# Kernel optimization log

Hardware: AMD Instinct MI355X
Metric: run time of the kernel (lower is better)

## Reference

```python
import jax, jax.numpy as jnp
import numpy as np

NUM_HEADS = 8
EPS = 1e-5  # torch GroupNorm default eps


def setup_inputs() -> dict:
    key = jax.random.key(0)
    ks = jax.random.split(key, 3)
    B, C, H, W = 8, 384, 32, 32
    x = jax.random.normal(ks[0], (B, C, H, W), dtype=jnp.float32)
    qkv_w = jax.random.normal(ks[1], (3 * C, C), dtype=jnp.float32) * 0.02
    proj_w = jax.random.normal(ks[2], (C, C), dtype=jnp.float32) * 0.02
    proj_b = jnp.zeros((C,), dtype=jnp.float32)
    lambda_param = jnp.ones((1, NUM_HEADS, 1, 1), dtype=jnp.float32) * 0.5
    gc = NUM_HEADS * ((C // NUM_HEADS) // 2)  # 192 group-norm channels
    gn_weight = jnp.ones((gc,), dtype=jnp.float32)
    gn_bias = jnp.zeros((gc,), dtype=jnp.float32)
    return {"x": x, "qkv_w": qkv_w, "lambda_param": lambda_param,
            "gn_weight": gn_weight, "gn_bias": gn_bias,
            "proj_w": proj_w, "proj_b": proj_b}


def reference(x, qkv_w, lambda_param, gn_weight, gn_bias, proj_w, proj_b):
    B, C, H, W = x.shape
    nh = NUM_HEADS
    hd = C // nh
    hd2 = hd // 2
    N = H * W
    scale = hd ** -0.5

    xf = x.reshape(B, C, N)
    qkv = jnp.einsum('oc,bcn->bon', qkv_w, xf)  # (B, 3C, N), 1x1 conv no bias
    q, k, v = jnp.split(qkv, 3, axis=1)
    q = q.reshape(B, nh, hd, N)
    k = k.reshape(B, nh, hd, N)
    v = v.reshape(B, nh, hd, N)

    q1, q2 = q[:, :, :hd2], q[:, :, hd2:]
    k1, k2 = k[:, :, :hd2], k[:, :, hd2:]
    v1, v2 = v[:, :, :hd2], v[:, :, hd2:]

    # GroupNorm(2 groups) on q2 viewed as (B, nh*hd2, H, W)
    gc = nh * hd2
    qg = q2.reshape(B, 2, (gc // 2) * N)  # normalize over (group channels, H, W)
    mean = qg.mean(axis=2, keepdims=True)
    var = qg.var(axis=2, keepdims=True)
    qg = (qg - mean) * jax.lax.rsqrt(var + EPS)
    q2n = qg.reshape(B, gc, N) * gn_weight[None, :, None] + gn_bias[None, :, None]
    q2n = q2n.reshape(B, nh, hd2, N)

    # dual softmax attention maps (B, nh, N, N)
    attn1 = jax.nn.softmax(jnp.einsum('bhdn,bhdm->bhnm', q1, k1) * scale, axis=-1)
    attn2 = jax.nn.softmax(jnp.einsum('bhdn,bhdm->bhnm', q2n, k2) * scale * lambda_param, axis=-1)
    diff = attn1 - attn2

    out1 = jnp.einsum('bhnm,bhdm->bhnd', diff, v1)  # (B, nh, N, hd2)
    out2 = jnp.einsum('bhnm,bhdm->bhnd', diff, v2)
    out = jnp.concatenate([out1, out2], axis=2)  # (B, nh, 2N, hd2) -- matches torch cat dim=2
    out = out.reshape(B, C, H, W)

    out = jnp.einsum('oc,bchw->bohw', proj_w, out) + proj_b[None, :, None, None]
    return out
```

## Files before the change

kernel.cpp:

```cpp
#include <hip/hip_runtime.h>
#include <hip/hip_bf16.h>
#include <stdint.h>

typedef _Float16 half8 __attribute__((ext_vector_type(8)));
typedef _Float16 half4 __attribute__((ext_vector_type(4)));
typedef __fp16 fp16x2 __attribute__((ext_vector_type(2)));
typedef float floatx4 __attribute__((ext_vector_type(4)));
typedef float floatx16 __attribute__((ext_vector_type(16)));

#define SCALE 0.14433756729740643f
#define LOG2E 1.4426950408889634f


__device__ inline float fexp2(float x) { return __builtin_exp2f(x); }

__device__ inline uint32_t pkrtz(float a, float b) {
  fp16x2 h = __builtin_amdgcn_cvt_pkrtz(a, b);
  union { fp16x2 h; uint32_t u; } cv; cv.h = h; return cv.u;
}

__global__ void k_pack(const float* __restrict__ src, _Float16* __restrict__ dst, int nchunks) {
  int cid = blockIdx.x * 256 + threadIdx.x;
  if (cid >= nchunks) return;
  int lane = cid & 63;
  int t = cid >> 6;
  int cb = t % 12;
  int g16 = t / 12;
  const float* s = src + (long)(g16 * 16 + (lane & 15)) * 384 + cb * 32 + (lane >> 4) * 8;
  floatx4 a = *(const floatx4*)s;
  floatx4 b = *(const floatx4*)(s + 4);
  half8 h;
  #pragma unroll
  for (int j = 0; j < 4; j++) { h[j] = (_Float16)a[j]; h[j+4] = (_Float16)b[j]; }
  *(half8*)(dst + (long)cid * 8) = h;
}

__launch_bounds__(256)
__global__ void k_tr(const float* __restrict__ src, _Float16* __restrict__ dst) {
  const int cblk = blockIdx.x, nseg = blockIdx.y, b = blockIdx.z;
  const float* S = src + ((long)b * 384 + cblk * 32) * 1024 + nseg * 256;
  _Float16* D = dst + (long)b * 393216 + cblk * 32768 + (long)nseg * 256 * 32;
  __shared__ _Float16 T[32][264];
  const int wv = threadIdx.x >> 6, lane = threadIdx.x & 63;
  #pragma unroll
  for (int rr = 0; rr < 8; rr++) {
    int r = wv * 8 + rr;
    floatx4 v = *(const floatx4*)(S + (long)r * 1024 + lane * 4);
    half4 h;
    #pragma unroll
    for (int j = 0; j < 4; j++) h[j] = (_Float16)v[j];
    *(half4*)&T[r][lane * 4] = h;
  }
  __syncthreads();
  const int nn = threadIdx.x >> 3, c = (threadIdx.x & 7) * 4;
  #pragma unroll
  for (int p = 0; p < 8; p++) {
    int n = p * 32 + nn;
    half4 h;
    #pragma unroll
    for (int i = 0; i < 4; i++) h[i] = T[c + i][n];
    *(half4*)(D + (long)n * 32 + c) = h;
  }
}

__launch_bounds__(256, 4)
__global__ void k_qkv(const _Float16* __restrict__ Xt, const _Float16* __restrict__ Wf,
                      _Float16* __restrict__ Qs, _Float16* __restrict__ Ks,
                      _Float16* __restrict__ Vs) {
  const int tid = threadIdx.x;
  const int lane = tid & 63;
  const int wv = tid >> 6;
  const int l15 = lane & 15;
  const int g = lane >> 4;
  const int o0 = blockIdx.x * 48;
  const int n0 = blockIdx.y * 64;
  const int b = blockIdx.z;

  const int ncol = n0 + wv * 16 + l15;
  const _Float16* xp = Xt + (long)b * 393216 + (long)ncol * 32 + g * 8;
  const _Float16* wfb = Wf + (long)(blockIdx.x * 36) * 512 + lane * 8;

  half8 xb[12];
  #pragma unroll
  for (int cb = 0; cb < 12; cb++) xb[cb] = *(const half8*)(xp + cb * 32768);

  floatx4 zero4 = {0.f, 0.f, 0.f, 0.f};
  floatx4 acc0 = zero4, acc1 = zero4, acc2 = zero4;

  half8 A0 = *(const half8*)(wfb);
  half8 A1 = *(const half8*)(wfb + 12 * 512);
  half8 A2 = *(const half8*)(wfb + 24 * 512);
  #pragma unroll
  for (int cb = 0; cb < 12; cb++) {
    half8 c0 = A0, c1 = A1, c2 = A2;
    if (cb < 11) {
      A0 = *(const half8*)(wfb + (cb + 1) * 512);
      A1 = *(const half8*)(wfb + (12 + cb + 1) * 512);
      A2 = *(const half8*)(wfb + (24 + cb + 1) * 512);
    }
    acc0 = __builtin_amdgcn_mfma_f32_16x16x32_f16(c0, xb[cb], acc0, 0, 0, 0);
    acc1 = __builtin_amdgcn_mfma_f32_16x16x32_f16(c1, xb[cb], acc1, 0, 0, 0);
    acc2 = __builtin_amdgcn_mfma_f32_16x16x32_f16(c2, xb[cb], acc2, 0, 0, 0);
  }

  floatx4 acc[3] = {acc0, acc1, acc2};
  __shared__ __align__(16) _Float16 T[3456];

  if (o0 < 768) {
    #pragma unroll
    for (int rt = 0; rt < 3; rt++)
      #pragma unroll
      for (int r = 0; r < 4; r++)
        T[(wv * 16 + l15) * 52 + rt * 16 + g * 4 + r] = (_Float16)acc[rt][r];
    __syncthreads();
    const int qk = o0 >= 384;
    const int hh = (o0 - qk * 384) / 48;
    _Float16* base = (qk ? Ks : Qs) + (long)(b * 8 + hh) * 65536;
    #pragma unroll
    for (int it = 0; it < 2; it++) {
      int slot = it * 256 + tid;
      int ntl = slot >> 8;
      int t   = (slot >> 6) & 3;
      int ln  = slot & 63;
      int hi_s = ln >> 5, l31_s = ln & 31;
      int n_ = ntl * 32 + l31_s;
      int c0 = t * 16 + hi_s * 8;
      half8 val;
      #pragma unroll
      for (int j = 0; j < 8; j++) {
        int col = c0 + j;
        int d48 = col < 24 ? col : col - 8;
        bool isq = (col < 24) || (col >= 32 && col < 56);
        val[j] = isq ? T[n_ * 52 + d48] : (_Float16)0;
      }
      *(half8*)(base + ((((n0 >> 5) + ntl) * 4 + t) * 64 + ln) * 8) = val;
    }
  } else {
    #pragma unroll
    for (int rt = 0; rt < 3; rt++)
      #pragma unroll
      for (int r = 0; r < 4; r++)
        T[(rt * 16 + g * 4 + r) * 72 + wv * 16 + l15] = (_Float16)acc[rt][r];
    __syncthreads();
    const int hh = (o0 - 768) / 48;
    _Float16* base = Vs + (long)(b * 8 + hh) * 65536;
    #pragma unroll
    for (int it = 0; it < 2; it++) {
      int slot = it * 256 + tid;
      int lwin = slot >> 8;
      int ckc  = (slot >> 6) & 3;
      int kc   = ckc & 1, c = ckc >> 1;
      int ln = slot & 63;
      int hi_s = ln >> 5, l31_s = ln & 31;
      int d48 = c * 32 + l31_s;
      half8 val;
      if (d48 < 48) {
        int mb = lwin * 32 + kc * 16 + hi_s * 4;
        half4 a = *(const half4*)&T[d48 * 72 + mb];
        half4 bq = *(const half4*)&T[d48 * 72 + mb + 8];
        val[0] = a[0]; val[1] = a[1]; val[2] = a[2]; val[3] = a[3];
        val[4] = bq[0]; val[5] = bq[1]; val[6] = bq[2]; val[7] = bq[3];
      } else {
        _Float16 f = (d48 == 48) ? (_Float16)1 : (_Float16)0;
        #pragma unroll
        for (int j = 0; j < 8; j++) val[j] = f;
      }
      *(half8*)(base + ((((n0 >> 5) + lwin) * 4 + ckc) * 64 + ln) * 8) = val;
    }
  }
}

__global__ void k_gnstats(const _Float16* __restrict__ Qs, float* __restrict__ partial) {
  int bg = blockIdx.x >> 3;
  int chunk = blockIdx.x & 7;
  int b = bg >> 1, grp = bg & 1;
  float s1 = 0.f, s2 = 0.f;
  #pragma unroll
  for (int k = 0; k < 6; k++) {
    int f = chunk * 1536 + k * 256 + threadIdx.x;
    int uid = f / 96;
    int slot = f - uid * 96;
    int h = grp * 4 + (uid >> 5);
    int ntile = uid & 31;
    int t = slot < 64 ? 2 : 3;
    int ln = slot < 64 ? slot : slot - 64;
    const _Float16* p = Qs + (long)(b * 8 + h) * 65536 + ((ntile * 4 + t) * 64 + ln) * 8;
    half8 v = *(const half8*)p;
    #pragma unroll
    for (int j = 0; j < 8; j++) { float x = (float)v[j]; s1 += x; s2 += x * x; }
  }
  #pragma unroll
  for (int off = 32; off > 0; off >>= 1) {
    s1 += __shfl_down(s1, off);
    s2 += __shfl_down(s2, off);
  }
  __shared__ float red[8];
  int wv = threadIdx.x >> 6;
  if ((threadIdx.x & 63) == 0) { red[wv] = s1; red[4 + wv] = s2; }
  __syncthreads();
  if (threadIdx.x == 0) {
    float S1 = red[0] + red[1] + red[2] + red[3];
    float S2 = red[4] + red[5] + red[6] + red[7];
    partial[blockIdx.x * 2]     = S1;
    partial[blockIdx.x * 2 + 1] = S2;
  }
}

__launch_bounds__(512, 4)
__global__ void k_attn(const _Float16* __restrict__ Qs, const _Float16* __restrict__ Ks,
                       const _Float16* __restrict__ Vs, const float* __restrict__ partial,
                       const float* __restrict__ lam, const float* __restrict__ gw,
                       const float* __restrict__ gb, float* __restrict__ Y) {
  const int tid = threadIdx.x;
  const int lane = tid & 63;
  const int wv = tid >> 6;
  const int l31 = lane & 31;
  const int hi = lane >> 5;
  const int id = blockIdx.x;
  const int bh = ((id >> 6) << 3) | (id & 7);
  const int ntlgrp = (id >> 3) & 7;
  const int br = wv & 1;
  const int ntile = ntlgrp * 4 + (wv >> 1);
  const int n0 = ntile * 32;
  const int b = bh >> 3, h = bh & 7;

  const _Float16* Qp = Qs + (long)bh * 65536 + (ntile * 256 + lane) * 8;
  half8 qra = *(const half8*)(Qp + (2 * br) * 512);
  half8 qrb = *(const half8*)(Qp + (2 * br + 1) * 512);
  half8 qfa, qfb;
  if (br == 0) {
    const float s1s = SCALE * LOG2E;
    #pragma unroll
    for (int j = 0; j < 8; j++) {
      qfa[j] = (_Float16)((float)qra[j] * s1s);
      qfb[j] = (_Float16)((float)qrb[j] * s1s);
    }
  } else {
    const int grp = h >> 2;
    const float* pp = partial + (b * 2 + grp) * 16;
    float S1 = 0.f, S2 = 0.f;
    #pragma unroll
    for (int i = 0; i < 8; i++) { S1 += pp[2*i]; S2 += pp[2*i+1]; }
    float mean = S1 * (1.f / 98304.f);
    float rstd = rsqrtf(S2 * (1.f / 98304.f) - mean * mean + 1e-5f);
    float sl = SCALE * LOG2E * lam[h];
    const float* gwp = gw + h * 24;
    const float* gbp = gb + h * 24;
    #pragma unroll
    for (int j = 0; j < 8; j++) {
      qfa[j] = (_Float16)((((float)qra[j] - mean) * rstd * gwp[hi * 8 + j] + gbp[hi * 8 + j]) * sl);
      qfb[j] = (_Float16)((((float)qrb[j] - mean) * rstd * gwp[16 + j] + gbp[16 + j]) * sl);
    }
  }

  const _Float16* gK = Ks + (long)bh * 65536 + ((wv >> 2) * 2048 + (wv & 3) * 512) + lane * 8;
  const _Float16* gV = Vs + (long)bh * 65536 + ((wv >> 2) * 2048 + (wv & 3) * 512) + lane * 8;

  __shared__ __align__(16) char smem[32768];
  const int ldsK = wv * 1024 + lane * 16;
  const int ldsV = 8192 + wv * 1024 + lane * 16;

  floatx16 z16;
  #pragma unroll
  for (int i = 0; i < 16; i++) z16[i] = 0.f;
  floatx16 accA = z16, accB = z16;

  {
    uint4 a = *(const uint4*)gK;
    uint4 c = *(const uint4*)gV;
    *(uint4*)(smem + ldsK) = a;
    *(uint4*)(smem + ldsV) = c;
  }
  __syncthreads();

  #pragma unroll 2
  for (int i = 0; i < 16; i++) {
    const int cur = (i & 1) << 14;
    uint4 sa, sc;
    if (i < 15) {
      sa = *(const uint4*)(gK + (i + 1) * 4096);
      sc = *(const uint4*)(gV + (i + 1) * 4096);
    }
    #pragma unroll
    for (int j = 0; j < 2; j++) {
      const char* Kb = smem + cur + j * 4096;
      const char* Vb = smem + cur + 8192 + j * 4096;
      half8 kfa = *(const half8*)(Kb + (2 * br) * 1024 + lane * 16);
      half8 kfb = *(const half8*)(Kb + (2 * br + 1) * 1024 + lane * 16);

      floatx16 s = __builtin_amdgcn_mfma_f32_32x32x16_f16(kfa, qfa, z16, 0, 0, 0);
      s = __builtin_amdgcn_mfma_f32_32x32x16_f16(kfb, qfb, s, 0, 0, 0);

      half8 vf0 = *(const half8*)(Vb + lane * 16);
      half8 vf1 = *(const half8*)(Vb + 1024 + lane * 16);
      half8 vf2 = *(const half8*)(Vb + 2048 + lane * 16);
      half8 vf3 = *(const half8*)(Vb + 3072 + lane * 16);

      uint32_t u[8];
      #pragma unroll
      for (int q = 0; q < 8; q++)
        u[q] = pkrtz(fexp2(s[2 * q]), fexp2(s[2 * q + 1]));

      union { uint32_t u[4]; half8 h; } pa;
      pa.u[0] = u[0]; pa.u[1] = u[1]; pa.u[2] = u[2]; pa.u[3] = u[3];
      half8 pc0 = pa.h;
      pa.u[0] = u[4]; pa.u[1] = u[5]; pa.u[2] = u[6]; pa.u[3] = u[7];
      half8 pc1 = pa.h;

      accA = __builtin_amdgcn_mfma_f32_32x32x16_f16(pc0, vf0, accA, 0, 0, 0);
      accA = __builtin_amdgcn_mfma_f32_32x32x16_f16(pc1, vf1, accA, 0, 0, 0);
      accB = __builtin_amdgcn_mfma_f32_32x32x16_f16(pc0, vf2, accB, 0, 0, 0);
      accB = __builtin_amdgcn_mfma_f32_32x32x16_f16(pc1, vf3, accB, 0, 0, 0);
    }
    if (i < 15) {
      *(uint4*)(smem + (cur ^ 16384) + ldsK) = sa;
      *(uint4*)(smem + (cur ^ 16384) + ldsV) = sc;
    }
    __syncthreads();
  }

  const int pairid = wv >> 1;
  float* rbuf = (float*)(smem + pairid * 8192);
  if (br == 1) {
    #pragma unroll
    for (int r = 0; r < 16; r++) {
      rbuf[r * 64 + lane] = accA[r];
      rbuf[(16 + r) * 64 + lane] = accB[r];
    }
  }
  __syncthreads();
  if (br == 0) {
    float a2a[16], a2b[16];
    #pragma unroll
    for (int r = 0; r < 16; r++) {
      a2a[r] = rbuf[r * 64 + lane];
      a2b[r] = rbuf[(16 + r) * 64 + lane];
    }
    float* Ybh = Y + (long)bh * 49152;
    const int src = (lane & 32) + 16;
    #pragma unroll
    for (int r = 0; r < 16; r++) {
      float i1 = __builtin_amdgcn_rcpf(__shfl(accB[r], src));
      float i2 = __builtin_amdgcn_rcpf(__shfl(a2b[r], src));
      int n = n0 + (r & 3) + 8 * ((r >> 2) & 3) + 4 * hi;
      float o0 = accA[r] * i1 - a2a[r] * i2;
      float o1 = accB[r] * i1 - a2b[r] * i2;
      int p0 = l31 >= 24;
      Ybh[p0 * 24576 + n * 24 + (l31 - p0 * 24)] = o0;
      if (l31 < 16) Ybh[24576 + n * 24 + 8 + l31] = o1;
    }
  }
}

__launch_bounds__(256, 4)
__global__ void k_proj(const _Float16* __restrict__ Yt, const _Float16* __restrict__ PWf,
                       const float* __restrict__ PB, float* __restrict__ out) {
  const int tid = threadIdx.x, lane = tid & 63, wv = tid >> 6, l15 = lane & 15, g = lane >> 4;
  const int o0 = blockIdx.x * 64, m0 = blockIdx.y * 64, b = blockIdx.z;

  const int mcol = m0 + wv * 16 + l15;
  const _Float16* yp = Yt + (long)b * 393216 + (long)mcol * 32 + g * 8;
  const _Float16* wfb = PWf + (long)(blockIdx.x * 48) * 512 + lane * 8;

  half8 yb[12];
  #pragma unroll
  for (int cb = 0; cb < 12; cb++) yb[cb] = *(const half8*)(yp + cb * 32768);

  floatx4 zero4 = {0.f, 0.f, 0.f, 0.f};
  floatx4 acc0 = zero4, acc1 = zero4, acc2 = zero4, acc3 = zero4;

  half8 A0 = *(const half8*)(wfb);
  half8 A1 = *(const half8*)(wfb + 12 * 512);
  half8 A2 = *(const half8*)(wfb + 24 * 512);
  half8 A3 = *(const half8*)(wfb + 36 * 512);
  #pragma unroll
  for (int cb = 0; cb < 12; cb++) {
    half8 c0 = A0, c1 = A1, c2 = A2, c3 = A3;
    if (cb < 11) {
      A0 = *(const half8*)(wfb + (cb + 1) * 512);
      A1 = *(const half8*)(wfb + (12 + cb + 1) * 512);
      A2 = *(const half8*)(wfb + (24 + cb + 1) * 512);
      A3 = *(const half8*)(wfb + (36 + cb + 1) * 512);
    }
    acc0 = __builtin_amdgcn_mfma_f32_16x16x32_f16(c0, yb[cb], acc0, 0, 0, 0);
    acc1 = __builtin_amdgcn_mfma_f32_16x16x32_f16(c1, yb[cb], acc1, 0, 0, 0);
    acc2 = __builtin_amdgcn_mfma_f32_16x16x32_f16(c2, yb[cb], acc2, 0, 0, 0);
    acc3 = __builtin_amdgcn_mfma_f32_16x16x32_f16(c3, yb[cb], acc3, 0, 0, 0);
  }

  floatx4 acc[4] = {acc0, acc1, acc2, acc3};
  #pragma unroll
  for (int rt = 0; rt < 4; rt++) {
    int o_ = o0 + rt * 16 + g * 4;
    #pragma unroll
    for (int r = 0; r < 4; r++) {
      out[(long)(b * 384 + o_ + r) * 1024 + mcol] = acc[rt][r] + PB[o_ + r];
    }
  }
}

extern "C" void kernel_launch(void* const* d_in, const int* in_sizes, int n_in,
                              void* d_out, int out_size, void* d_ws, size_t ws_size,
                              hipStream_t stream) {
  const float* x     = (const float*)d_in[0];
  const float* qkv_w = (const float*)d_in[1];
  const float* lam   = (const float*)d_in[2];
  const float* gw    = (const float*)d_in[3];
  const float* gb    = (const float*)d_in[4];
  const float* pw    = (const float*)d_in[5];
  const float* pb    = (const float*)d_in[6];
  float* out = (float*)d_out;
  char* ws = (char*)d_ws;
  _Float16* Qs  = (_Float16*)ws;
  _Float16* Ks  = (_Float16*)(ws + 8388608);
  _Float16* Vs  = (_Float16*)(ws + 16777216);
  float* Y        = (float*)(ws + 25165824);
  float* partial  = (float*)(ws + 37748736);
  _Float16* Xt  = (_Float16*)(ws + 37752832);
  _Float16* Yt  = (_Float16*)(ws + 44044288);
  _Float16* Wf  = (_Float16*)(ws + 50335744);
  _Float16* PWf = (_Float16*)(ws + 51220480);

  hipLaunchKernelGGL(k_pack,    dim3(216),        dim3(256), 0, stream, qkv_w, Wf, 55296);
  hipLaunchKernelGGL(k_pack,    dim3(72),         dim3(256), 0, stream, pw, PWf, 18432);
  hipLaunchKernelGGL(k_tr,      dim3(12, 4, 8),   dim3(256), 0, stream, x, Xt);
  hipLaunchKernelGGL(k_qkv,     dim3(24, 16, 8),  dim3(256), 0, stream, Xt, Wf, Qs, Ks, Vs);
  hipLaunchKernelGGL(k_gnstats, dim3(128),        dim3(256), 0, stream, Qs, partial);
  hipLaunchKernelGGL(k_attn,    dim3(512),        dim3(512), 0, stream, Qs, Ks, Vs, partial, lam, gw, gb, Y);
  hipLaunchKernelGGL(k_tr,      dim3(12, 4, 8),   dim3(256), 0, stream, Y, Yt);
  hipLaunchKernelGGL(k_proj,    dim3(6, 16, 8),   dim3(256), 0, stream, Yt, PWf, pb, out);
}
```

Measured before the change: 102.3 us.

## Split attention key range across wave pairs and fuse prep kernels into one launch

The attention kernel now launches twice as many blocks, each covering two query tiles instead of four. Waves are split into two halves over the key dimension, and the two partial accumulators are combined through LDS before the dual-softmax combine. The goal is more parallelism and occupancy for the attention stage, with launch bounds raised from 4 to 6. In exchange it adds an extra LDS reduction and barrier, puts more register pressure under the tighter bound, and the key loop is still split into only 16 iterations. Separately, the two weight-pack launches and the input-transpose launch are merged into one kernel to cut launch overhead.

```diff
diff --git a/kernel.cpp b/kernel.cpp
--- a/kernel.cpp
+++ b/kernel.cpp
@@ -19,20 +19,55 @@
   union { fp16x2 h; uint32_t u; } cv; cv.h = h; return cv.u;
 }
 
-__global__ void k_pack(const float* __restrict__ src, _Float16* __restrict__ dst, int nchunks) {
-  int cid = blockIdx.x * 256 + threadIdx.x;
-  if (cid >= nchunks) return;
-  int lane = cid & 63;
-  int t = cid >> 6;
-  int cb = t % 12;
-  int g16 = t / 12;
-  const float* s = src + (long)(g16 * 16 + (lane & 15)) * 384 + cb * 32 + (lane >> 4) * 8;
-  floatx4 a = *(const floatx4*)s;
-  floatx4 b = *(const floatx4*)(s + 4);
-  half8 h;
-  #pragma unroll
-  for (int j = 0; j < 4; j++) { h[j] = (_Float16)a[j]; h[j+4] = (_Float16)b[j]; }
-  *(half8*)(dst + (long)cid * 8) = h;
+__launch_bounds__(256)
+__global__ void k_prep(const float* __restrict__ qkv_w, const float* __restrict__ pw,
+                       const float* __restrict__ x, _Float16* __restrict__ Wf,
+                       _Float16* __restrict__ PWf, _Float16* __restrict__ Xt) {
+  const int bid = blockIdx.x;
+  if (bid < 288) {
+    const float* src = (bid < 216) ? qkv_w : pw;
+    _Float16* dst = (bid < 216) ? Wf : PWf;
+    int cid = (bid < 216 ? bid : bid - 216) * 256 + threadIdx.x;
+    int nchunks = (bid < 216) ? 55296 : 18432;
+    if (cid >= nchunks) return;
+    int lane = cid & 63;
+    int t = cid >> 6;
+    int cb = t % 12;
+    int g16 = t / 12;
+    const float* s = src + (long)(g16 * 16 + (lane & 15)) * 384 + cb * 32 + (lane >> 4) * 8;
+    floatx4 a = *(const floatx4*)s;
+    floatx4 b = *(const floatx4*)(s + 4);
+    half8 h;
+    #pragma unroll
+    for (int j = 0; j < 4; j++) { h[j] = (_Float16)a[j]; h[j+4] = (_Float16)b[j]; }
+    *(half8*)(dst + (long)cid * 8) = h;
+  } else {
+    int idx = bid - 288;
+    const int cblk = idx % 12, nseg = (idx / 12) & 3, b = idx / 48;
+    const float* S = x + ((long)b * 384 + cblk * 32) * 1024 + nseg * 256;
+    _Float16* D = Xt + (long)b * 393216 + cblk * 32768 + (long)nseg * 256 * 32;
+    __shared__ _Float16 T[32][264];
+    const int wv = threadIdx.x >> 6, lane = threadIdx.x & 63;
+    #pragma unroll
+    for (int rr = 0; rr < 8; rr++) {
+      int r = wv * 8 + rr;
+      floatx4 v = *(const floatx4*)(S + (long)r * 1024 + lane * 4);
+      half4 h;
+      #pragma unroll
+      for (int j = 0; j < 4; j++) h[j] = (_Float16)v[j];
+      *(half4*)&T[r][lane * 4] = h;
+    }
+    __syncthreads();
+    const int nn = threadIdx.x >> 3, c = (threadIdx.x & 7) * 4;
+    #pragma unroll
+    for (int p = 0; p < 8; p++) {
+      int n = p * 32 + nn;
+      half4 h;
+      #pragma unroll
+      for (int i = 0; i < 4; i++) h[i] = T[c + i][n];
+      *(half4*)(D + (long)n * 32 + c) = h;
+    }
+  }
 }
 
 __launch_bounds__(256)
@@ -206,7 +241,7 @@
   }
 }
 
-__launch_bounds__(512, 4)
+__launch_bounds__(512, 6)
 __global__ void k_attn(const _Float16* __restrict__ Qs, const _Float16* __restrict__ Ks,
                        const _Float16* __restrict__ Vs, const float* __restrict__ partial,
                        const float* __restrict__ lam, const float* __restrict__ gw,
@@ -217,10 +252,12 @@
   const int l31 = lane & 31;
   const int hi = lane >> 5;
   const int id = blockIdx.x;
-  const int bh = ((id >> 6) << 3) | (id & 7);
-  const int ntlgrp = (id >> 3) & 7;
-  const int br = wv & 1;
-  const int ntile = ntlgrp * 4 + (wv >> 1);
+  const int bh = ((id >> 7) << 3) | (id & 7);
+  const int ntpair = (id >> 3) & 15;
+  const int kh  = wv & 1;
+  const int br  = (wv >> 1) & 1;
+  const int ntl = wv >> 2;
+  const int ntile = ntpair * 2 + ntl;
   const int n0 = ntile * 32;
   const int b = bh >> 3, h = bh & 7;
 
@@ -253,8 +290,8 @@
     }
   }
 
-  const _Float16* gK = Ks + (long)bh * 65536 + ((wv >> 2) * 2048 + (wv & 3) * 512) + lane * 8;
-  const _Float16* gV = Vs + (long)bh * 65536 + ((wv >> 2) * 2048 + (wv & 3) * 512) + lane * 8;
+  const _Float16* gK = Ks + (long)bh * 65536 + (wv >> 2) * 32768 + (wv & 3) * 512 + lane * 8;
+  const _Float16* gV = Vs + (long)bh * 65536 + (wv >> 2) * 32768 + (wv & 3) * 512 + lane * 8;
 
   __shared__ __align__(16) char smem[32768];
   const int ldsK = wv * 1024 + lane * 16;
@@ -278,40 +315,38 @@
     const int cur = (i & 1) << 14;
     uint4 sa, sc;
     if (i < 15) {
-      sa = *(const uint4*)(gK + (i + 1) * 4096);
-      sc = *(const uint4*)(gV + (i + 1) * 4096);
-    }
-    #pragma unroll
-    for (int j = 0; j < 2; j++) {
-      const char* Kb = smem + cur + j * 4096;
-      const char* Vb = smem + cur + 8192 + j * 4096;
-      half8 kfa = *(const half8*)(Kb + (2 * br) * 1024 + lane * 16);
-      half8 kfb = *(const half8*)(Kb + (2 * br + 1) * 1024 + lane * 16);
-
-      floatx16 s = __builtin_amdgcn_mfma_f32_32x32x16_f16(kfa, qfa, z16, 0, 0, 0);
-      s = __builtin_amdgcn_mfma_f32_32x32x16_f16(kfb, qfb, s, 0, 0, 0);
-
-      half8 vf0 = *(const half8*)(Vb + lane * 16);
-      half8 vf1 = *(const half8*)(Vb + 1024 + lane * 16);
-      half8 vf2 = *(const half8*)(Vb + 2048 + lane * 16);
-      half8 vf3 = *(const half8*)(Vb + 3072 + lane * 16);
-
-      uint32_t u[8];
-      #pragma unroll
-      for (int q = 0; q < 8; q++)
-        u[q] = pkrtz(fexp2(s[2 * q]), fexp2(s[2 * q + 1]));
-
-      union { uint32_t u[4]; half8 h; } pa;
-      pa.u[0] = u[0]; pa.u[1] = u[1]; pa.u[2] = u[2]; pa.u[3] = u[3];
-      half8 pc0 = pa.h;
-      pa.u[0] = u[4]; pa.u[1] = u[5]; pa.u[2] = u[6]; pa.u[3] = u[7];
-      half8 pc1 = pa.h;
-
-      accA = __builtin_amdgcn_mfma_f32_32x32x16_f16(pc0, vf0, accA, 0, 0, 0);
-      accA = __builtin_amdgcn_mfma_f32_32x32x16_f16(pc1, vf1, accA, 0, 0, 0);
-      accB = __builtin_amdgcn_mfma_f32_32x32x16_f16(pc0, vf2, accB, 0, 0, 0);
-      accB = __builtin_amdgcn_mfma_f32_32x32x16_f16(pc1, vf3, accB, 0, 0, 0);
-    }
+      sa = *(const uint4*)(gK + (i + 1) * 2048);
+      sc = *(const uint4*)(gV + (i + 1) * 2048);
+    }
+    const char* Kb = smem + cur + kh * 4096;
+    const char* Vb = smem + cur + 8192 + kh * 4096;
+    half8 kfa = *(const half8*)(Kb + (2 * br) * 1024 + lane * 16);
+    half8 kfb = *(const half8*)(Kb + (2 * br + 1) * 1024 + lane * 16);
+
+    floatx16 s = __builtin_amdgcn_mfma_f32_32x32x16_f16(kfa, qfa, z16, 0, 0, 0);
+    s = __builtin_amdgcn_mfma_f32_32x32x16_f16(kfb, qfb, s, 0, 0, 0);
+
+    half8 vf0 = *(const half8*)(Vb + lane * 16);
+    half8 vf1 = *(const half8*)(Vb + 1024 + lane * 16);
+    half8 vf2 = *(const half8*)(Vb + 2048 + lane * 16);
+    half8 vf3 = *(const half8*)(Vb + 3072 + lane * 16);
+
+    uint32_t u[8];
+    #pragma unroll
+    for (int q = 0; q < 8; q++)
+      u[q] = pkrtz(fexp2(s[2 * q]), fexp2(s[2 * q + 1]));
+
+    union { uint32_t u[4]; half8 h; } pa;
+    pa.u[0] = u[0]; pa.u[1] = u[1]; pa.u[2] = u[2]; pa.u[3] = u[3];
+    half8 pc0 = pa.h;
+    pa.u[0] = u[4]; pa.u[1] = u[5]; pa.u[2] = u[6]; pa.u[3] = u[7];
+    half8 pc1 = pa.h;
+
+    accA = __builtin_amdgcn_mfma_f32_32x32x16_f16(pc0, vf0, accA, 0, 0, 0);
+    accA = __builtin_amdgcn_mfma_f32_32x32x16_f16(pc1, vf1, accA, 0, 0, 0);
+    accB = __builtin_amdgcn_mfma_f32_32x32x16_f16(pc0, vf2, accB, 0, 0, 0);
+    accB = __builtin_amdgcn_mfma_f32_32x32x16_f16(pc1, vf3, accB, 0, 0, 0);
+
     if (i < 15) {
       *(uint4*)(smem + (cur ^ 16384) + ldsK) = sa;
       *(uint4*)(smem + (cur ^ 16384) + ldsV) = sc;
@@ -319,32 +354,47 @@
     __syncthreads();
   }
 
-  const int pairid = wv >> 1;
-  float* rbuf = (float*)(smem + pairid * 8192);
-  if (br == 1) {
+  {
+    float* rbuf = (float*)(smem + (wv >> 1) * 8192);
+    if (kh == 1) {
+      #pragma unroll
+      for (int r = 0; r < 16; r++) {
+        rbuf[r * 64 + lane] = accA[r];
+        rbuf[(16 + r) * 64 + lane] = accB[r];
+      }
+    }
+    __syncthreads();
+    if (kh == 0) {
+      #pragma unroll
+      for (int r = 0; r < 16; r++) {
+        accA[r] += rbuf[r * 64 + lane];
+        accB[r] += rbuf[(16 + r) * 64 + lane];
+      }
+    }
+    __syncthreads();
+  }
+
+  float* rbuf2 = (float*)(smem + (wv >> 2) * 8192);
+  if (kh == 0 && br == 1) {
     #pragma unroll
     for (int r = 0; r < 16; r++) {
-      rbuf[r * 64 + lane] = accA[r];
-      rbuf[(16 + r) * 64 + lane] = accB[r];
+      rbuf2[r * 64 + lane] = accA[r];
+      rbuf2[(16 + r) * 64 + lane] = accB[r];
     }
   }
   __syncthreads();
-  if (br == 0) {
-    float a2a[16], a2b[16];
-    #pragma unroll
-    for (int r = 0; r < 16; r++) {
-      a2a[r] = rbuf[r * 64 + lane];
-      a2b[r] = rbuf[(16 + r) * 64 + lane];
-    }
+  if (kh == 0 && br == 0) {
     float* Ybh = Y + (long)bh * 49152;
     const int src = (lane & 32) + 16;
     #pragma unroll
     for (int r = 0; r < 16; r++) {
+      float a2a = rbuf2[r * 64 + lane];
+      float a2b = rbuf2[(16 + r) * 64 + lane];
       float i1 = __builtin_amdgcn_rcpf(__shfl(accB[r], src));
-      float i2 = __builtin_amdgcn_rcpf(__shfl(a2b[r], src));
+      float i2 = __builtin_amdgcn_rcpf(__shfl(a2b, src));
       int n = n0 + (r & 3) + 8 * ((r >> 2) & 3) + 4 * hi;
-      float o0 = accA[r] * i1 - a2a[r] * i2;
-      float o1 = accB[r] * i1 - a2b[r] * i2;
+      float o0 = accA[r] * i1 - a2a * i2;
+      float o1 = accB[r] * i1 - a2b * i2;
       int p0 = l31 >= 24;
       Ybh[p0 * 24576 + n * 24 + (l31 - p0 * 24)] = o0;
       if (l31 < 16) Ybh[24576 + n * 24 + 8 + l31] = o1;
@@ -421,12 +471,10 @@
   _Float16* Wf  = (_Float16*)(ws + 50335744);
   _Float16* PWf = (_Float16*)(ws + 51220480);
 
-  hipLaunchKernelGGL(k_pack,    dim3(216),        dim3(256), 0, stream, qkv_w, Wf, 55296);
-  hipLaunchKernelGGL(k_pack,    dim3(72),         dim3(256), 0, stream, pw, PWf, 18432);
-  hipLaunchKernelGGL(k_tr,      dim3(12, 4, 8),   dim3(256), 0, stream, x, Xt);
+  hipLaunchKernelGGL(k_prep,    dim3(672),        dim3(256), 0, stream, qkv_w, pw, x, Wf, PWf, Xt);
   hipLaunchKernelGGL(k_qkv,     dim3(24, 16, 8),  dim3(256), 0, stream, Xt, Wf, Qs, Ks, Vs);
   hipLaunchKernelGGL(k_gnstats, dim3(128),        dim3(256), 0, stream, Qs, partial);
-  hipLaunchKernelGGL(k_attn,    dim3(512),        dim3(512), 0, stream, Qs, Ks, Vs, partial, lam, gw, gb, Y);
+  hipLaunchKernelGGL(k_attn,    dim3(1024),       dim3(512), 0, stream, Qs, Ks, Vs, partial, lam, gw, gb, Y);
   hipLaunchKernelGGL(k_tr,      dim3(12, 4, 8),   dim3(256), 0, stream, Y, Yt);
   hipLaunchKernelGGL(k_proj,    dim3(6, 16, 8),   dim3(256), 0, stream, Yt, PWf, pb, out);
 }
```

Measured after the change: 112.3 us. 9.8% more time.
